# Performance work log

Hardware: AMD Instinct MI355X
Metric: run time of the kernel (lower is better)

The kernel has to match this reference:

```python
import jax, jax.numpy as jnp
import numpy as np

B, N, C, K = 8, 4096, 256, 8192

def setup_inputs() -> dict:
    key = jax.random.key(0)
    k1, k2 = jax.random.split(key)
    z_e_x = jax.random.normal(k1, (B, N, C), dtype=jnp.float32)
    # codebook initialized like the torch module: normal(0,1) rescaled so mean row norm = sqrt(D)
    cb = jax.random.normal(k2, (K, C), dtype=jnp.float32)
    cur = jnp.mean(jnp.linalg.norm(cb, axis=1))
    cb = cb * (jnp.sqrt(jnp.float32(C)) / cur)
    return {"z_e_x": z_e_x, "codebook": cb}

def reference(z_e_x, codebook):
    """VQ straight-through forward: returns (codes, idx, distances).
    codes: [B,N,C] nearest codebook vectors; idx: [B,N] int32 indices;
    distances: [B,N] min squared L2 distances."""
    b, n, c = z_e_x.shape
    x = z_e_x.astype(jnp.float32).reshape(b * n, c)          # [BN, C]
    cb = codebook.astype(jnp.float32)                        # [K, C]
    cb_sq = jnp.sum(cb * cb, axis=1)                         # [K]
    x_sq = jnp.sum(x * x, axis=1, keepdims=True)             # [BN,1]
    l2 = x_sq + cb_sq[None, :] - 2.0 * (x @ cb.T)            # [BN, K]
    idx_flat = jnp.argmin(l2, axis=1)                        # [BN]
    min_vals = jnp.min(l2, axis=1)                           # [BN]
    codes = jnp.take(cb, idx_flat, axis=0).reshape(b, n, c).astype(z_e_x.dtype)
    idx = idx_flat.reshape(b, n)
    distances = min_vals.reshape(b, n).astype(z_e_x.dtype)
    return codes, idx, distances
```

## Files before the change

kernel.cpp:

```cpp
#include <hip/hip_runtime.h>
#include <hip/hip_bf16.h>
#include <stdint.h>


#define M_ROWS 32768
#define KCODES 8192
#define CDIM   256
#define BM 128
#define BNT 256
#define BK 32
#define NTILES 32
#define NREC 32
#define MARGIN 0.75f

typedef _Float16 f16x8 __attribute__((ext_vector_type(8)));
typedef _Float16 f16x4 __attribute__((ext_vector_type(4)));
typedef float    f32x4 __attribute__((ext_vector_type(4)));

#define WAITV(N) asm volatile("s_waitcnt vmcnt(" #N ")" ::: "memory")

__device__ __forceinline__ unsigned umin2(unsigned a, unsigned b) { return a < b ? a : b; }
__device__ __forceinline__ unsigned umax2(unsigned a, unsigned b) { return a > b ? a : b; }

__global__ void vq_prep(const float* __restrict__ x, const float* __restrict__ cb,
                        _Float16* __restrict__ xhi, _Float16* __restrict__ cbhi,
                        float* __restrict__ xsq, float* __restrict__ cbsq) {
  const int wave = threadIdx.x >> 6, lane = threadIdx.x & 63;
  const int row = blockIdx.x * 4 + wave;
  const float* src;
  _Float16* dhi;
  float* dsq;
  if (row < M_ROWS) {
    src = x + (size_t)row * CDIM;  dhi = xhi + (size_t)row * CDIM;  dsq = xsq + row;
  } else {
    const int r = row - M_ROWS;
    src = cb + (size_t)r * CDIM;   dhi = cbhi + (size_t)r * CDIM;   dsq = cbsq + r;
  }
  const float4 v = *(const float4*)(src + lane * 4);
  f16x4 h;
  h[0] = (_Float16)(v.x * 64.0f); h[1] = (_Float16)(v.y * 64.0f);
  h[2] = (_Float16)(v.z * 64.0f); h[3] = (_Float16)(v.w * 64.0f);
  *(f16x4*)(dhi + lane * 4) = h;
  float s = v.x * v.x + v.y * v.y + v.z * v.z + v.w * v.w;
  #pragma unroll
  for (int off = 32; off > 0; off >>= 1) s += __shfl_down(s, off, 64);
  if (lane == 0) *dsq = s;
}

__device__ __forceinline__ void gl16p(const void* g, void* l) {
  __builtin_amdgcn_global_load_lds(
      (const __attribute__((address_space(1))) unsigned int*)g,
      (__attribute__((address_space(3))) unsigned int*)l, 16, 0, 0);
}

__global__ __launch_bounds__(512) void vq_pass1(
    const _Float16* __restrict__ xhi, const _Float16* __restrict__ cbhi,
    const float* __restrict__ cbsqg, uint2* __restrict__ srec) {
  extern __shared__ char smem[];
  _Float16* sA = (_Float16*)smem;
  _Float16* sB = (_Float16*)(smem + 65536);

  const int tid  = threadIdx.x;
  const int wave = tid >> 6, lane = tid & 63;
  const int quad = lane >> 4, l15 = lane & 15;
  const int mbase = blockIdx.x * BM;
  const int wrow = (wave >> 2) * 64;
  const int q    = wave & 3;
  const int wcol = q * 64;

  {
    const int ar = lane >> 5;
    const int as = lane & 31;
    #pragma unroll
    for (int t = 0; t < 8; ++t) {
      const int rb  = (wave * 8 + t) * 2;
      const int row = rb + ar;
      const int slot = as ^ (row & 7);
      gl16p(xhi + (size_t)(mbase + row) * CDIM + slot * 8, sA + rb * CDIM);
    }
  }

  const int srl  = lane >> 2;
  const int scol = (((lane & 3) ^ ((lane >> 3) & 3)) << 3);
  const int fcol = ((quad ^ ((l15 >> 1) & 3)) << 3);
  const int asw  = l15 & 7;

  _Float16* sBw = sB + wave * 4096;

  auto stageB = [&](int nts, int kss, int buf) {
    const int c0 = nts * BNT + wcol;
    const int kofs = kss * BK;
    _Float16* dst = sBw + buf * 2048;
    #pragma unroll
    for (int t = 0; t < 4; ++t)
      gl16p(cbhi + (size_t)(c0 + t * 16 + srl) * CDIM + kofs + scol, dst + t * 512);
  };

  float cq_cur[4], cq_nxt[4];
  #pragma unroll
  for (int j = 0; j < 4; ++j) cq_cur[j] = cbsqg[wcol + j * 16 + l15];

  stageB(0, 0, 0);
  WAITV(4);
  __builtin_amdgcn_s_barrier();
  asm volatile("" ::: "memory");

  unsigned k1[4][4], k2[4][4];

  for (int nt = 0; nt < NTILES; ++nt) {
    const bool lastnt = (nt == NTILES - 1);
    if ((nt & 3) == 0) {
      #pragma unroll
      for (int mf = 0; mf < 4; ++mf)
        #pragma unroll
        for (int i = 0; i < 4; ++i) { k1[mf][i] = 0x7fffffffu; k2[mf][i] = 0x7fffffffu; }
    }

    f32x4 acc[4][4];
    #pragma unroll
    for (int mf = 0; mf < 4; ++mf)
      #pragma unroll
      for (int nf = 0; nf < 4; ++nf) {
        f32x4 z = {0.0f, 0.0f, 0.0f, 0.0f};
        acc[mf][nf] = z;
      }

    #pragma unroll
    for (int ks = 0; ks < 8; ++ks) {
      WAITV(0);
      asm volatile("" ::: "memory");
      if (ks < 7)        stageB(nt, ks + 1, (ks + 1) & 1);
      else if (!lastnt)  stageB(nt + 1, 0, 0);
      if (ks == 6 && !lastnt) {
        #pragma unroll
        for (int j = 0; j < 4; ++j)
          cq_nxt[j] = cbsqg[(nt + 1) * BNT + wcol + j * 16 + l15];
      }

      const _Float16* sBc = sBw + (ks & 1) * 2048;
      const int aslot = (ks * 4 + quad) ^ asw;
      f16x8 ah[4];
      #pragma unroll
      for (int mf = 0; mf < 4; ++mf)
        ah[mf] = *(const f16x8*)(sA + (wrow + mf * 16 + l15) * CDIM + aslot * 8);
      __builtin_amdgcn_s_setprio(1);
      #pragma unroll
      for (int nf = 0; nf < 4; ++nf) {
        const f16x8 bh = *(const f16x8*)(sBc + (nf * 16 + l15) * BK + fcol);
        #pragma unroll
        for (int mf = 0; mf < 4; ++mf)
          acc[mf][nf] = __builtin_amdgcn_mfma_f32_16x16x32_f16(ah[mf], bh, acc[mf][nf], 0, 0, 0);
      }
      __builtin_amdgcn_s_setprio(0);
    }

    #pragma unroll
    for (int nf = 0; nf < 4; ++nf) {
      const int col = nt * BNT + wcol + nf * 16 + l15;
      const float cq16 = fmaf(cq_cur[nf], 16.0f, 32768.0f);
      #pragma unroll
      for (int mf = 0; mf < 4; ++mf)
        #pragma unroll
        for (int i = 0; i < 4; ++i) {
          const float kf = fmaf(acc[mf][nf][i], -0.0078125f, cq16);
          const unsigned key = ((unsigned)kf << 13) | (unsigned)col;
          k2[mf][i] = umin2(k2[mf][i], umax2(k1[mf][i], key));
          k1[mf][i] = umin2(k1[mf][i], key);
        }
    }

    if ((nt & 3) == 3) {
      const int g = (nt >> 2) * 4 + q;
      #pragma unroll
      for (int mf = 0; mf < 4; ++mf)
        #pragma unroll
        for (int i = 0; i < 4; ++i) {
          unsigned a1 = k1[mf][i], a2 = k2[mf][i];
          #pragma unroll
          for (int m = 1; m <= 8; m <<= 1) {
            const unsigned o1 = (unsigned)__shfl_xor((int)a1, m, 64);
            const unsigned o2 = (unsigned)__shfl_xor((int)a2, m, 64);
            a2 = umin2(umin2(a2, o2), umax2(a1, o1));
            a1 = umin2(a1, o1);
          }
          if (l15 == 0) {
            const int rl = wrow + mf * 16 + quad * 4 + i;
            uint2 r; r.x = a1; r.y = a2;
            srec[(size_t)(mbase + rl) * NREC + g] = r;
          }
        }
    }

    #pragma unroll
    for (int j = 0; j < 4; ++j) cq_cur[j] = cq_nxt[j];
  }
}

__global__ void vq_finalize(const float* __restrict__ x, const float* __restrict__ cb,
                            const float* __restrict__ xsq, const float* __restrict__ cbsq,
                            const uint2* __restrict__ srec,
                            float* __restrict__ outIdx, float* __restrict__ outDist,
                            float* __restrict__ codes) {
  const int wave = threadIdx.x >> 6, lane = threadIdx.x & 63;
  const int row = blockIdx.x * 4 + wave;
  uint2 rec;
  if (lane < NREC) rec = srec[(size_t)row * NREC + lane];
  else { rec.x = 0x7fffffffu; rec.y = 0x7fffffffu; }
  const float v1 = (float)(rec.x >> 13) * 0.0625f - 2048.0f;
  const float v2 = (float)(rec.y >> 13) * 0.0625f - 2048.0f;
  const int c1 = (int)(rec.x & 8191u);
  const int c2 = (int)(rec.y & 8191u);

  float gm = v1;
  #pragma unroll
  for (int m = 1; m <= 32; m <<= 1) gm = fminf(gm, __shfl_xor(gm, m, 64));
  const float thr = gm + MARGIN;
  unsigned long long mask1 = __ballot(v1 <= thr);
  unsigned long long mask2 = __ballot(v2 <= thr);

  const float4 xv = *(const float4*)(x + (size_t)row * CDIM + lane * 4);
  const float xq = xsq[row];
  float best = __builtin_inff(); int bidx = 1 << 30;

  #pragma unroll
  for (int pass = 0; pass < 2; ++pass) {
    unsigned long long m = pass ? mask2 : mask1;
    const int fi = pass ? c2 : c1;
    while (m) {
      const int g = __builtin_ctzll((long long)m); m &= m - 1;
      const int ci = __shfl(fi, g, 64);
      const float4 cv = *(const float4*)(cb + (size_t)ci * CDIM + lane * 4);
      float s = xv.x * cv.x + xv.y * cv.y + xv.z * cv.z + xv.w * cv.w;
      #pragma unroll
      for (int mm = 1; mm <= 32; mm <<= 1) s += __shfl_xor(s, mm, 64);
      const float dist = xq + cbsq[ci] - 2.0f * s;
      if (dist < best || (dist == best && ci < bidx)) { best = dist; bidx = ci; }
    }
  }

  if (lane == 0) { outIdx[row] = (float)bidx; outDist[row] = best; }
  const float4 cw = *(const float4*)(cb + (size_t)bidx * CDIM + lane * 4);
  *(float4*)(codes + (size_t)row * CDIM + lane * 4) = cw;
}

extern "C" void kernel_launch(void* const* d_in, const int* in_sizes, int n_in,
                              void* d_out, int out_size, void* d_ws, size_t ws_size,
                              hipStream_t stream) {
  const float* x  = (const float*)d_in[0];
  const float* cb = (const float*)d_in[1];
  float* out = (float*)d_out;

  char* w = (char*)d_ws;
  _Float16* xhi  = (_Float16*)(w);
  _Float16* cbhi = (_Float16*)(w + 16777216);
  float*    xsq  = (float*)   (w + 20971520);
  float*    cbsq = (float*)   (w + 21102592);
  uint2*    srec = (uint2*)   (w + 21135360);

  vq_prep<<<(M_ROWS + KCODES) / 4, 256, 0, stream>>>(x, cb, xhi, cbhi, xsq, cbsq);
  const size_t smem = 65536 + 65536;
  vq_pass1<<<dim3(M_ROWS / BM), 512, smem, stream>>>(xhi, cbhi, cbsq, srec);
  vq_finalize<<<M_ROWS / 4, 256, 0, stream>>>(x, cb, xsq, cbsq, srec,
                                              out + 8388608, out + 8421376, out);
}
```

Baseline: 279.4 us.

## Hold A fragments in registers, deepen B prefetch, stage codebook norms in LDS

The X tile fragments are now loaded once into registers (32 f16x8 per lane) rather than staged in LDS and re-read every k-step, which frees LDS. That space is used for a 4-buffer ring per wave, so codebook tiles are prefetched two k-steps ahead and the wait only drains the older loads. All codebook squared norms are copied into LDS up front, replacing the per-tile global reloads. The cost is higher register pressure (waves_per_eu hint 1-2) and 160KB of LDS per block.

Measured after the change: 326.7 us. +16.9%, slower.

```diff
diff --git a/kernel.cpp b/kernel.cpp
--- a/kernel.cpp
+++ b/kernel.cpp
@@ -53,12 +53,13 @@
       (__attribute__((address_space(3))) unsigned int*)l, 16, 0, 0);
 }
 
-__global__ __launch_bounds__(512) void vq_pass1(
+__global__ __launch_bounds__(512) __attribute__((amdgpu_waves_per_eu(1, 2)))
+void vq_pass1(
     const _Float16* __restrict__ xhi, const _Float16* __restrict__ cbhi,
     const float* __restrict__ cbsqg, uint2* __restrict__ srec) {
   extern __shared__ char smem[];
-  _Float16* sA = (_Float16*)smem;
-  _Float16* sB = (_Float16*)(smem + 65536);
+  _Float16* sB  = (_Float16*)smem;
+  float*    sCq = (float*)(smem + 131072);
 
   const int tid  = threadIdx.x;
   const int wave = tid >> 6, lane = tid & 63;
@@ -68,24 +69,11 @@
   const int q    = wave & 3;
   const int wcol = q * 64;
 
-  {
-    const int ar = lane >> 5;
-    const int as = lane & 31;
-    #pragma unroll
-    for (int t = 0; t < 8; ++t) {
-      const int rb  = (wave * 8 + t) * 2;
-      const int row = rb + ar;
-      const int slot = as ^ (row & 7);
-      gl16p(xhi + (size_t)(mbase + row) * CDIM + slot * 8, sA + rb * CDIM);
-    }
-  }
-
   const int srl  = lane >> 2;
   const int scol = (((lane & 3) ^ ((lane >> 3) & 3)) << 3);
   const int fcol = ((quad ^ ((l15 >> 1) & 3)) << 3);
-  const int asw  = l15 & 7;
-
-  _Float16* sBw = sB + wave * 4096;
+
+  _Float16* sBw = sB + wave * 8192;
 
   auto stageB = [&](int nts, int kss, int buf) {
     const int c0 = nts * BNT + wcol;
@@ -96,12 +84,26 @@
       gl16p(cbhi + (size_t)(c0 + t * 16 + srl) * CDIM + kofs + scol, dst + t * 512);
   };
 
-  float cq_cur[4], cq_nxt[4];
-  #pragma unroll
-  for (int j = 0; j < 4; ++j) cq_cur[j] = cbsqg[wcol + j * 16 + l15];
-
+  f16x8 aF[4][8];
+  #pragma unroll
+  for (int mf = 0; mf < 4; ++mf) {
+    const _Float16* arow = xhi + (size_t)(mbase + wrow + mf * 16 + l15) * CDIM;
+    #pragma unroll
+    for (int kk = 0; kk < 8; ++kk)
+      aF[mf][kk] = *(const f16x8*)(arow + kk * 32 + quad * 8);
+  }
+  asm volatile("" ::: "memory");
+
+  {
+    const float* srcq = cbsqg + wave * 1024;
+    float* dstq = sCq + wave * 1024;
+    #pragma unroll
+    for (int t = 0; t < 4; ++t)
+      gl16p(srcq + t * 256 + lane * 4, dstq + t * 256);
+  }
   stageB(0, 0, 0);
-  WAITV(4);
+  stageB(0, 1, 1);
+  WAITV(8);
   __builtin_amdgcn_s_barrier();
   asm volatile("" ::: "memory");
 
@@ -127,37 +129,31 @@
 
     #pragma unroll
     for (int ks = 0; ks < 8; ++ks) {
-      WAITV(0);
+      if (ks == 7 && lastnt) { WAITV(0); } else { WAITV(4); }
       asm volatile("" ::: "memory");
-      if (ks < 7)        stageB(nt, ks + 1, (ks + 1) & 1);
-      else if (!lastnt)  stageB(nt + 1, 0, 0);
-      if (ks == 6 && !lastnt) {
-        #pragma unroll
-        for (int j = 0; j < 4; ++j)
-          cq_nxt[j] = cbsqg[(nt + 1) * BNT + wcol + j * 16 + l15];
+      if (ks <= 5)            stageB(nt, ks + 2, (ks + 2) & 3);
+      else if (!lastnt) {
+        if (ks == 6)          stageB(nt + 1, 0, 0);
+        else                  stageB(nt + 1, 1, 1);
       }
 
-      const _Float16* sBc = sBw + (ks & 1) * 2048;
-      const int aslot = (ks * 4 + quad) ^ asw;
-      f16x8 ah[4];
-      #pragma unroll
-      for (int mf = 0; mf < 4; ++mf)
-        ah[mf] = *(const f16x8*)(sA + (wrow + mf * 16 + l15) * CDIM + aslot * 8);
+      const _Float16* sBc = sBw + (ks & 3) * 2048;
       __builtin_amdgcn_s_setprio(1);
       #pragma unroll
       for (int nf = 0; nf < 4; ++nf) {
         const f16x8 bh = *(const f16x8*)(sBc + (nf * 16 + l15) * BK + fcol);
         #pragma unroll
         for (int mf = 0; mf < 4; ++mf)
-          acc[mf][nf] = __builtin_amdgcn_mfma_f32_16x16x32_f16(ah[mf], bh, acc[mf][nf], 0, 0, 0);
+          acc[mf][nf] = __builtin_amdgcn_mfma_f32_16x16x32_f16(aF[mf][ks], bh, acc[mf][nf], 0, 0, 0);
       }
       __builtin_amdgcn_s_setprio(0);
     }
 
     #pragma unroll
     for (int nf = 0; nf < 4; ++nf) {
-      const int col = nt * BNT + wcol + nf * 16 + l15;
-      const float cq16 = fmaf(cq_cur[nf], 16.0f, 32768.0f);
+      const int cwl = wcol + nf * 16 + l15;
+      const int col = nt * BNT + cwl;
+      const float cq16 = fmaf(sCq[col], 16.0f, 32768.0f);
       #pragma unroll
       for (int mf = 0; mf < 4; ++mf)
         #pragma unroll
@@ -190,9 +186,6 @@
           }
         }
     }
-
-    #pragma unroll
-    for (int j = 0; j < 4; ++j) cq_cur[j] = cq_nxt[j];
   }
 }
 
@@ -258,7 +251,7 @@
   uint2*    srec = (uint2*)   (w + 21135360);
 
   vq_prep<<<(M_ROWS + KCODES) / 4, 256, 0, stream>>>(x, cb, xhi, cbhi, xsq, cbsq);
-  const size_t smem = 65536 + 65536;
+  const size_t smem = 131072 + 32768;
   vq_pass1<<<dim3(M_ROWS / BM), 512, smem, stream>>>(xhi, cbhi, cbsq, srec);
   vq_finalize<<<M_ROWS / 4, 256, 0, stream>>>(x, cb, xsq, cbsq, srec,
                                               out + 8388608, out + 8421376, out);
```

## Triple-buffer per-wave codebook staging and stagger half the waves

Applied to the files above, without the earlier changes.

Switches the per-wave B-tile LDS staging from double to triple buffering with a rotating buffer index, so loads run two k-steps ahead and each step waits on vmcnt(8) instead of draining all loads. Shared memory grows to 160KB, and the launch attribute now allows up to two waves per EU. Waves 4-7 sleep briefly at the start so the two halves of the block go out of phase and MFMA bursts overlap better. The larger LDS footprint limits occupancy to one block per CU, and the vmcnt accounting on the final tile is fragile.

Measured after the change: 280.8 us. Within noise of the previous version (+0.5%).

```diff
diff --git a/kernel.cpp b/kernel.cpp
--- a/kernel.cpp
+++ b/kernel.cpp
@@ -53,7 +53,8 @@
       (__attribute__((address_space(3))) unsigned int*)l, 16, 0, 0);
 }
 
-__global__ __launch_bounds__(512) void vq_pass1(
+__global__ __attribute__((amdgpu_flat_work_group_size(512, 512), amdgpu_waves_per_eu(1, 2)))
+void vq_pass1(
     const _Float16* __restrict__ xhi, const _Float16* __restrict__ cbhi,
     const float* __restrict__ cbsqg, uint2* __restrict__ srec) {
   extern __shared__ char smem[];
@@ -85,25 +86,28 @@
   const int fcol = ((quad ^ ((l15 >> 1) & 3)) << 3);
   const int asw  = l15 & 7;
 
-  _Float16* sBw = sB + wave * 4096;
-
-  auto stageB = [&](int nts, int kss, int buf) {
+  _Float16* sBw = sB + wave * 6144;
+
+  auto stageB = [&](int nts, int kss, int offs) {
     const int c0 = nts * BNT + wcol;
     const int kofs = kss * BK;
-    _Float16* dst = sBw + buf * 2048;
+    _Float16* dst = sBw + offs;
     #pragma unroll
     for (int t = 0; t < 4; ++t)
       gl16p(cbhi + (size_t)(c0 + t * 16 + srl) * CDIM + kofs + scol, dst + t * 512);
   };
 
+  stageB(0, 0, 0);
+  stageB(0, 1, 2048);
   float cq_cur[4], cq_nxt[4];
   #pragma unroll
   for (int j = 0; j < 4; ++j) cq_cur[j] = cbsqg[wcol + j * 16 + l15];
-
-  stageB(0, 0, 0);
-  WAITV(4);
+  WAITV(12);
   __builtin_amdgcn_s_barrier();
   asm volatile("" ::: "memory");
+  if (wave & 4) { asm volatile("s_sleep 10"); }
+
+  int r0 = 0, r1 = 2048, r2 = 4096;
 
   unsigned k1[4][4], k2[4][4];
 
@@ -127,17 +131,29 @@
 
     #pragma unroll
     for (int ks = 0; ks < 8; ++ks) {
-      WAITV(0);
-      asm volatile("" ::: "memory");
-      if (ks < 7)        stageB(nt, ks + 1, (ks + 1) & 1);
-      else if (!lastnt)  stageB(nt + 1, 0, 0);
-      if (ks == 6 && !lastnt) {
-        #pragma unroll
-        for (int j = 0; j < 4; ++j)
-          cq_nxt[j] = cbsqg[(nt + 1) * BNT + wcol + j * 16 + l15];
+      if (ks <= 5) {
+        stageB(nt, ks + 2, r2);
+        WAITV(8);
+      } else if (ks == 6) {
+        if (!lastnt) {
+          stageB(nt + 1, 0, r2);
+          #pragma unroll
+          for (int j = 0; j < 4; ++j)
+            cq_nxt[j] = cbsqg[(nt + 1) * BNT + wcol + j * 16 + l15];
+          WAITV(12);
+        } else {
+          WAITV(4);
+        }
+      } else {
+        if (!lastnt) {
+          stageB(nt + 1, 1, r2);
+          WAITV(8);
+        } else {
+          WAITV(0);
+        }
       }
 
-      const _Float16* sBc = sBw + (ks & 1) * 2048;
+      const _Float16* sBc = sBw + r0;
       const int aslot = (ks * 4 + quad) ^ asw;
       f16x8 ah[4];
       #pragma unroll
@@ -152,6 +168,8 @@
           acc[mf][nf] = __builtin_amdgcn_mfma_f32_16x16x32_f16(ah[mf], bh, acc[mf][nf], 0, 0, 0);
       }
       __builtin_amdgcn_s_setprio(0);
+
+      { const int tmp = r0; r0 = r1; r1 = r2; r2 = tmp; }
     }
 
     #pragma unroll
@@ -258,7 +276,7 @@
   uint2*    srec = (uint2*)   (w + 21135360);
 
   vq_prep<<<(M_ROWS + KCODES) / 4, 256, 0, stream>>>(x, cb, xhi, cbhi, xsq, cbsq);
-  const size_t smem = 65536 + 65536;
+  const size_t smem = 65536 + 98304;
   vq_pass1<<<dim3(M_ROWS / BM), 512, smem, stream>>>(xhi, cbhi, cbsq, srec);
   vq_finalize<<<M_ROWS / 4, 256, 0, stream>>>(x, cb, xsq, cbsq, srec,
                                               out + 8388608, out + 8421376, out);
```

## Deepen codebook prefetch pipeline and use med3 for top-2 selection

Applied to the files above, without the earlier changes.

The codebook staging is reworked to issue the next global-to-LDS load before waiting, using partial vmcnt waits instead of a full drain each k-step. Address arithmetic moves to precomputed byte offsets incremented per step, and each wave's LDS region is padded. The top-2 key update is replaced with v_med3_u32, which cuts the min/max instruction count in the epilogue and the shuffle reduction. The risk is in the hand-tuned waitcnt counts and offset constants, which must exactly match the number of loads in flight.

New measurement: 288.2 us. 3.2% more time.

```diff
diff --git a/kernel.cpp b/kernel.cpp
--- a/kernel.cpp
+++ b/kernel.cpp
@@ -18,9 +18,14 @@
 typedef float    f32x4 __attribute__((ext_vector_type(4)));
 
 #define WAITV(N) asm volatile("s_waitcnt vmcnt(" #N ")" ::: "memory")
+#define CPIN()   asm volatile("" ::: "memory")
 
 __device__ __forceinline__ unsigned umin2(unsigned a, unsigned b) { return a < b ? a : b; }
-__device__ __forceinline__ unsigned umax2(unsigned a, unsigned b) { return a > b ? a : b; }
+__device__ __forceinline__ unsigned umed3(unsigned a, unsigned b, unsigned c) {
+  unsigned d;
+  asm("v_med3_u32 %0, %1, %2, %3" : "=v"(d) : "v"(a), "v"(b), "v"(c));
+  return d;
+}
 
 __global__ void vq_prep(const float* __restrict__ x, const float* __restrict__ cb,
                         _Float16* __restrict__ xhi, _Float16* __restrict__ cbhi,
@@ -58,7 +63,7 @@
     const float* __restrict__ cbsqg, uint2* __restrict__ srec) {
   extern __shared__ char smem[];
   _Float16* sA = (_Float16*)smem;
-  _Float16* sB = (_Float16*)(smem + 65536);
+  char* sBb = smem + 65536;
 
   const int tid  = threadIdx.x;
   const int wave = tid >> 6, lane = tid & 63;
@@ -79,31 +84,43 @@
       gl16p(xhi + (size_t)(mbase + row) * CDIM + slot * 8, sA + rb * CDIM);
     }
   }
+  CPIN();
 
   const int srl  = lane >> 2;
   const int scol = (((lane & 3) ^ ((lane >> 3) & 3)) << 3);
   const int fcol = ((quad ^ ((l15 >> 1) & 3)) << 3);
   const int asw  = l15 & 7;
 
-  _Float16* sBw = sB + wave * 4096;
-
-  auto stageB = [&](int nts, int kss, int buf) {
-    const int c0 = nts * BNT + wcol;
-    const int kofs = kss * BK;
-    _Float16* dst = sBw + buf * 2048;
-    #pragma unroll
-    for (int t = 0; t < 4; ++t)
-      gl16p(cbhi + (size_t)(c0 + t * 16 + srl) * CDIM + kofs + scol, dst + t * 512);
+  char* sBw = sBb + wave * 8224;
+
+  unsigned v0 = (unsigned)((wcol +  0 + srl) * 512 + scol * 2);
+  unsigned v1 = v0 + 16 * 512;
+  unsigned v2 = v0 + 32 * 512;
+  unsigned v3 = v0 + 48 * 512;
+
+  auto stage4 = [&](int buf) {
+    char* dst = sBw + buf * 4096;
+    const char* base = (const char*)cbhi;
+    gl16p(base + v0, dst);
+    gl16p(base + v1, dst + 1024);
+    gl16p(base + v2, dst + 2048);
+    gl16p(base + v3, dst + 3072);
   };
 
+  stage4(0);
+  CPIN();
   float cq_cur[4], cq_nxt[4];
   #pragma unroll
   for (int j = 0; j < 4; ++j) cq_cur[j] = cbsqg[wcol + j * 16 + l15];
-
-  stageB(0, 0, 0);
-  WAITV(4);
+  CPIN();
+  WAITV(8);
   __builtin_amdgcn_s_barrier();
-  asm volatile("" ::: "memory");
+  CPIN();
+  v0 += 64; v1 += 64; v2 += 64; v3 += 64;
+
+  const char* sArow = (const char*)sA + (wrow + l15) * 512;
+  const char* bB0 = sBw + l15 * 64 + fcol * 2;
+  const char* bB1 = bB0 + 4096;
 
   unsigned k1[4][4], k2[4][4];
 
@@ -127,29 +144,39 @@
 
     #pragma unroll
     for (int ks = 0; ks < 8; ++ks) {
-      WAITV(0);
-      asm volatile("" ::: "memory");
-      if (ks < 7)        stageB(nt, ks + 1, (ks + 1) & 1);
-      else if (!lastnt)  stageB(nt + 1, 0, 0);
-      if (ks == 6 && !lastnt) {
+      if (ks < 7) {
+        stage4((ks + 1) & 1);
+        if (ks == 6) { v0 += 130624; v1 += 130624; v2 += 130624; v3 += 130624; }
+        else         { v0 += 64;     v1 += 64;     v2 += 64;     v3 += 64;     }
+      } else if (!lastnt) {
+        stage4(0);
+        CPIN();
         #pragma unroll
         for (int j = 0; j < 4; ++j)
           cq_nxt[j] = cbsqg[(nt + 1) * BNT + wcol + j * 16 + l15];
+        v0 += 64; v1 += 64; v2 += 64; v3 += 64;
       }
-
-      const _Float16* sBc = sBw + (ks & 1) * 2048;
-      const int aslot = (ks * 4 + quad) ^ asw;
-      f16x8 ah[4];
-      #pragma unroll
-      for (int mf = 0; mf < 4; ++mf)
-        ah[mf] = *(const f16x8*)(sA + (wrow + mf * 16 + l15) * CDIM + aslot * 8);
+      if (ks == 0)       WAITV(8);
+      else if (ks < 7)   WAITV(4);
+      else if (!lastnt)  WAITV(8);
+      else               WAITV(0);
+      CPIN();
+
+      const int aoff = (((ks * 4 + quad) ^ asw) << 4);
+      const char* ab = sArow + aoff;
+      f16x8 ah0 = *(const f16x8*)(ab);
+      f16x8 ah1 = *(const f16x8*)(ab + 8192);
+      f16x8 ah2 = *(const f16x8*)(ab + 16384);
+      f16x8 ah3 = *(const f16x8*)(ab + 24576);
+      const char* bb = (ks & 1) ? bB1 : bB0;
       __builtin_amdgcn_s_setprio(1);
       #pragma unroll
       for (int nf = 0; nf < 4; ++nf) {
-        const f16x8 bh = *(const f16x8*)(sBc + (nf * 16 + l15) * BK + fcol);
-        #pragma unroll
-        for (int mf = 0; mf < 4; ++mf)
-          acc[mf][nf] = __builtin_amdgcn_mfma_f32_16x16x32_f16(ah[mf], bh, acc[mf][nf], 0, 0, 0);
+        const f16x8 bh = *(const f16x8*)(bb + nf * 1024);
+        acc[0][nf] = __builtin_amdgcn_mfma_f32_16x16x32_f16(ah0, bh, acc[0][nf], 0, 0, 0);
+        acc[1][nf] = __builtin_amdgcn_mfma_f32_16x16x32_f16(ah1, bh, acc[1][nf], 0, 0, 0);
+        acc[2][nf] = __builtin_amdgcn_mfma_f32_16x16x32_f16(ah2, bh, acc[2][nf], 0, 0, 0);
+        acc[3][nf] = __builtin_amdgcn_mfma_f32_16x16x32_f16(ah3, bh, acc[3][nf], 0, 0, 0);
       }
       __builtin_amdgcn_s_setprio(0);
     }
@@ -164,7 +191,7 @@
         for (int i = 0; i < 4; ++i) {
           const float kf = fmaf(acc[mf][nf][i], -0.0078125f, cq16);
           const unsigned key = ((unsigned)kf << 13) | (unsigned)col;
-          k2[mf][i] = umin2(k2[mf][i], umax2(k1[mf][i], key));
+          k2[mf][i] = umed3(k1[mf][i], k2[mf][i], key);
           k1[mf][i] = umin2(k1[mf][i], key);
         }
     }
@@ -180,7 +207,7 @@
           for (int m = 1; m <= 8; m <<= 1) {
             const unsigned o1 = (unsigned)__shfl_xor((int)a1, m, 64);
             const unsigned o2 = (unsigned)__shfl_xor((int)a2, m, 64);
-            a2 = umin2(umin2(a2, o2), umax2(a1, o1));
+            a2 = umin2(umin2(a2, o2), umed3(a1, a2, o1));
             a1 = umin2(a1, o1);
           }
           if (l15 == 0) {
@@ -258,7 +285,7 @@
   uint2*    srec = (uint2*)   (w + 21135360);
 
   vq_prep<<<(M_ROWS + KCODES) / 4, 256, 0, stream>>>(x, cb, xhi, cbhi, xsq, cbsq);
-  const size_t smem = 65536 + 65536;
+  const size_t smem = 65536 + 65792;
   vq_pass1<<<dim3(M_ROWS / BM), 512, smem, stream>>>(xhi, cbhi, cbsq, srec);
   vq_finalize<<<M_ROWS / 4, 256, 0, stream>>>(x, cb, xsq, cbsq, srec,
                                               out + 8388608, out + 8421376, out);
```
